# Kernel tuning notes

Measured on AMD Instinct MI355X. Metric: run time of the kernel, lower is better.

The kernel has to match this reference:

```python
import jax, jax.numpy as jnp
import numpy as np

B, T, I, H = 64, 188, 512, 1024
R = H  # recurrent_size == hidden_size (required for the cell math to be consistent)


def setup_inputs() -> dict:
    key = jax.random.key(0)
    ks = jax.random.split(key, 6)
    stdv = 1.0 / np.sqrt(H)
    u = lambda k, shape: jax.random.uniform(k, shape, jnp.float32, -stdv, stdv)
    return {
        "x": jax.random.normal(ks[0], (B, T, I), jnp.float32),
        "h0": jnp.zeros((B, R), jnp.float32),
        "c0": jnp.zeros((B, H), jnp.float32),
        "weight_ih": u(ks[1], (4 * H, I)),
        "weight_hh": u(ks[2], (4 * H, R)),
        "weight_rec": u(ks[3], (2 * R, H)),
        "bias": u(ks[4], (4 * H,)),
        "lengths": jax.random.randint(ks[5], (B,), 1, T + 1),
    }


def reference(x, h0, c0, weight_ih, weight_hh, weight_rec, bias, lengths):
    # length_matrix[j][t] == 1 iff t < lengths[j]; state is zeroed where 0
    mask = (jnp.arange(T)[:, None] < lengths[None, :]).astype(x.dtype)[:, :, None]  # [T,B,1]
    # precompute input projections for all timesteps: [T, B, 4H]
    pre_x = jnp.einsum('bti,gi->tbg', x, weight_ih) + bias

    def step(carry, inp):
        h, c = carry
        px, m = inp
        pre = px + h @ weight_hh.T           # [B, 4H]
        pre_c = c @ weight_rec.T             # [B, 2R] (peephole)
        i = jax.nn.sigmoid(pre[:, :H] + pre_c[:, :H])
        f = jax.nn.sigmoid(pre[:, H:2 * H] + pre_c[:, H:2 * H])
        g = jnp.tanh(pre[:, 2 * H:3 * H])
        c_new = f * c + i * g
        o = jax.nn.sigmoid(pre[:, 3 * H:] + c_new)
        h_new = o * jnp.tanh(c_new)
        h_new = h_new * m  # zero finished sequences (index_fill_ with 0)
        c_new = c_new * m
        return (h_new, c_new), (h_new, c_new)

    (_, _), (hs, cs) = jax.lax.scan(step, (h0, c0), (pre_x, mask))
    # stack over time then transpose(0,1) as in torch -> [B, T, H]
    return jnp.swapaxes(hs, 0, 1), jnp.swapaxes(cs, 0, 1)
```

## Files before the change

### kernel.cpp

```cpp
#include <hip/hip_runtime.h>


#define T_N 188

#define WS_PX     0UL
#define WS_XB     98566144UL
#define WS_WIHB   110886912UL
#define WS_WCOMB  115081216UL
#define WS_HST    127664128UL
#define WS_CST    127926272UL
#define WS_FLAGS  128188416UL
#define WS_WRECLO 128192512UL
#define WS_CSTLO  132386816UL

typedef __attribute__((ext_vector_type(8))) short short8;
typedef __attribute__((ext_vector_type(4))) float f4;

__device__ __forceinline__ float b2f(unsigned short u) {
    union { unsigned int i; float f; } v; v.i = ((unsigned int)u) << 16; return v.f;
}
__device__ __forceinline__ unsigned short f2b(float f) {
    unsigned int u = __float_as_uint(f);
    return (unsigned short)((u + 0x7FFFu + ((u >> 16) & 1u)) >> 16);
}
__device__ __forceinline__ float sigf(float x) { return 1.0f / (1.0f + __expf(-x)); }
__device__ __forceinline__ float tanh_(float x) {
    float e = __expf(2.0f * x); return 1.0f - 2.0f / (e + 1.0f);
}
#define MFMA(a, b, c) __builtin_amdgcn_mfma_f32_16x16x32_bf16((a), (b), (c), 0, 0, 0)

#define LD16(dst, addr) \
    asm volatile("global_load_dwordx4 %0, %1, off sc0 sc1" : "=&v"(dst) : "v"(addr))

__device__ __forceinline__ f4 px_init(const unsigned short* px, int t, int gate, int jg, int brow) {
    unsigned long long pv =
        *(const unsigned long long*)(px + ((long)(t * 4 + gate) * 1024 + jg) * 64 + brow);
    f4 r;
    r[0] = b2f((unsigned short)pv);
    r[1] = b2f((unsigned short)(pv >> 16));
    r[2] = b2f((unsigned short)(pv >> 32));
    r[3] = b2f((unsigned short)(pv >> 48));
    return r;
}

__global__ void k_prep(const float* __restrict__ x, const float* __restrict__ h0,
                       const float* __restrict__ c0, const float* __restrict__ wih,
                       const float* __restrict__ whh, const float* __restrict__ wrec,
                       unsigned short* __restrict__ xb, unsigned short* __restrict__ wihb,
                       unsigned short* __restrict__ wcomb, unsigned short* __restrict__ hst,
                       unsigned short* __restrict__ cst, unsigned short* __restrict__ wreclo,
                       unsigned short* __restrict__ cstlo, int* __restrict__ flags) {
    const long NX4 = 1540096, NWIH4 = 524288, NWHH4 = 1048576, NWREC4 = 524288, NH4 = 16384;
    const long total = NX4 + NWIH4 + NWHH4 + NWREC4 + NH4 + NH4;
    long gtid = (long)blockIdx.x * blockDim.x + threadIdx.x;
    for (long i = gtid; i < total; i += (long)gridDim.x * blockDim.x) {
        const float* src; unsigned short* dst; unsigned short* lo_dst = nullptr; long off = i;
        if (off < NX4)                   { src = x;    dst = xb; }
        else if ((off -= NX4) < NWIH4)   { src = wih;  dst = wihb; }
        else if ((off -= NWIH4) < NWHH4) { src = whh;  dst = wcomb; }
        else if ((off -= NWHH4) < NWREC4){ src = wrec; dst = wcomb + 4194304; lo_dst = wreclo; }
        else if ((off -= NWREC4) < NH4)  { src = h0;   dst = hst + 65536; }
        else { off -= NH4;                 src = c0;   dst = cst + 65536; lo_dst = cstlo + 65536; }
        float4 v = ((const float4*)src)[off];
        unsigned short hx = f2b(v.x), hy = f2b(v.y), hz = f2b(v.z), hw = f2b(v.w);
        unsigned long long o = (unsigned long long)hx
            | ((unsigned long long)hy << 16)
            | ((unsigned long long)hz << 32)
            | ((unsigned long long)hw << 48);
        *(unsigned long long*)(dst + off * 4) = o;
        if (lo_dst) {
            unsigned long long l = (unsigned long long)f2b(v.x - b2f(hx))
                | ((unsigned long long)f2b(v.y - b2f(hy)) << 16)
                | ((unsigned long long)f2b(v.z - b2f(hz)) << 32)
                | ((unsigned long long)f2b(v.w - b2f(hw)) << 48);
            *(unsigned long long*)(lo_dst + off * 4) = l;
        }
    }
    if (gtid < 1024) flags[gtid] = 0;
}

__global__ void __launch_bounds__(256) k_px(const unsigned short* __restrict__ xb,
                                            const unsigned short* __restrict__ wihb,
                                            const float* __restrict__ bias,
                                            unsigned short* __restrict__ px) {
    const int t = blockIdx.y;
    const int wv = threadIdx.x >> 6, lane = threadIdx.x & 63;
    const int col = lane & 15, quad = lane >> 4;
    const int n = blockIdx.x * 64 + wv * 16 + col;
    const float bn = bias[n];
    f4 acc[4];
#pragma unroll
    for (int mt = 0; mt < 4; ++mt) { acc[mt][0] = bn; acc[mt][1] = bn; acc[mt][2] = bn; acc[mt][3] = bn; }
    const unsigned short* bp = wihb + n * 512 + quad * 8;
#pragma unroll 4
    for (int kk = 0; kk < 16; ++kk) {
        short8 bf = *(const short8*)(bp + kk * 32);
#pragma unroll
        for (int mt = 0; mt < 4; ++mt) {
            const unsigned short* ap = xb + ((mt * 16 + col) * 188 + t) * 512 + kk * 32 + quad * 8;
            short8 af = *(const short8*)ap;
            acc[mt] = MFMA(af, bf, acc[mt]);
        }
    }
    const long pb = ((long)(t * 4 + (n >> 10)) * 1024 + (n & 1023)) * 64;
#pragma unroll
    for (int mt = 0; mt < 4; ++mt) {
        unsigned long long o = (unsigned long long)f2b(acc[mt][0])
            | ((unsigned long long)f2b(acc[mt][1]) << 16)
            | ((unsigned long long)f2b(acc[mt][2]) << 32)
            | ((unsigned long long)f2b(acc[mt][3]) << 48);
        *(unsigned long long*)(px + pb + mt * 16 + quad * 4) = o;
    }
}

__global__ void __launch_bounds__(256, 1) k_scan(
    const unsigned short* __restrict__ wcomb, const unsigned short* __restrict__ wreclo,
    const float* __restrict__ c0, const int* __restrict__ lengths,
    const unsigned short* __restrict__ px, unsigned short* __restrict__ hst,
    unsigned short* __restrict__ cst, unsigned short* __restrict__ cstlo,
    int* __restrict__ flags, float* __restrict__ out) {
    const int cu = blockIdx.x;
    const int g = cu >> 6, cig = cu & 63;
    const int jbase = cig * 16, b0 = g * 16;
    const int tid = threadIdx.x, wv = tid >> 6, lane = tid & 63;
    const int kh = wv >> 1, ts = wv & 1;
    const int kbase = kh * 512;
    const int col = lane & 15, quad = lane >> 4;

    __shared__ float pre[2][2][6][16][16];
    __shared__ float c_loc[16][16];

    short8 wf[4][16];
#pragma unroll
    for (int tile = 0; tile < 4; ++tile) {
        const unsigned short* src;
        if (ts == 0) {
            src = wcomb + (long)(tile * 1024 + jbase + col) * 1024 + kbase + quad * 8;
        } else if (tile < 2) {
            src = wcomb + (long)((4 + tile) * 1024 + jbase + col) * 1024 + kbase + quad * 8;
        } else {
            src = wreclo + (long)((tile - 2) * 1024 + jbase + col) * 1024 + kbase + quad * 8;
        }
#pragma unroll
        for (int kk = 0; kk < 16; ++kk) wf[tile][kk] = *(const short8*)(src + kk * 32);
    }
    {
        int b = tid >> 4, j = tid & 15;
        c_loc[b][j] = c0[(b0 + b) * 1024 + jbase + j];
    }
    const int my_len = lengths[b0 + (tid >> 4)];
    __syncthreads();

    float* out_h = out;
    float* out_c = out + 12320768;

    for (int t = 0; t < T_N; ++t) {
        const int sl_r = (t + 1) & 1, sl_w = t & 1, ps = t & 1;

        f4 pxv[4];
        if (ts == 0 && kh == 0) {
#pragma unroll
            for (int tile = 0; tile < 4; ++tile)
                pxv[tile] = px_init(px, t, tile, jbase + col, b0 + quad * 4);
        }

        if (t > 0) {
            if (wv == 0) {
                const int* fp = flags + g * 64 + lane;
                for (;;) {
                    int a = __hip_atomic_load(fp, __ATOMIC_RELAXED, __HIP_MEMORY_SCOPE_AGENT);
                    if (__all(a >= t)) break;
                    __builtin_amdgcn_s_sleep(1);
                }
            }
            __syncthreads();
            asm volatile("" ::: "memory");
        }

        const int sbase = sl_r * 65536 + (b0 + col) * 1024 + kbase + quad * 8;

        if (ts == 0) {
            const unsigned short* hp = hst + sbase;
            short8 hbuf[16];
#pragma unroll
            for (int kk = 0; kk < 16; ++kk) LD16(hbuf[kk], hp + kk * 32);
            f4 acc[4];
#pragma unroll
            for (int tile = 0; tile < 4; ++tile) {
                if (kh == 0) acc[tile] = pxv[tile];
                else { acc[tile][0] = 0.f; acc[tile][1] = 0.f; acc[tile][2] = 0.f; acc[tile][3] = 0.f; }
            }
            asm volatile("s_waitcnt vmcnt(0)" ::: "memory");
            __builtin_amdgcn_sched_barrier(0);
#pragma unroll
            for (int kk = 0; kk < 16; ++kk) {
                acc[0] = MFMA(hbuf[kk], wf[0][kk], acc[0]);
                acc[1] = MFMA(hbuf[kk], wf[1][kk], acc[1]);
                acc[2] = MFMA(hbuf[kk], wf[2][kk], acc[2]);
                acc[3] = MFMA(hbuf[kk], wf[3][kk], acc[3]);
            }
#pragma unroll
            for (int tile = 0; tile < 4; ++tile)
#pragma unroll
                for (int r = 0; r < 4; ++r) pre[ps][kh][tile][quad * 4 + r][col] = acc[tile][r];
        } else {
            const unsigned short* cph = cst + sbase;
            const unsigned short* cpl = cstlo + sbase;
            short8 chb[16], clb[16];
#pragma unroll
            for (int kk = 0; kk < 16; ++kk) LD16(chb[kk], cph + kk * 32);
#pragma unroll
            for (int kk = 0; kk < 16; ++kk) LD16(clb[kk], cpl + kk * 32);
            f4 a0 = {0.f, 0.f, 0.f, 0.f}, a1 = a0, a2 = a0, a3 = a0, a4 = a0, a5 = a0;
            asm volatile("s_waitcnt vmcnt(0)" ::: "memory");
            __builtin_amdgcn_sched_barrier(0);
#pragma unroll
            for (int kk = 0; kk < 16; ++kk) {
                a0 = MFMA(chb[kk], wf[0][kk], a0);
                a1 = MFMA(chb[kk], wf[1][kk], a1);
                a2 = MFMA(chb[kk], wf[2][kk], a2);
                a3 = MFMA(chb[kk], wf[3][kk], a3);
                a4 = MFMA(clb[kk], wf[0][kk], a4);
                a5 = MFMA(clb[kk], wf[1][kk], a5);
            }
#pragma unroll
            for (int r = 0; r < 4; ++r) {
                pre[ps][kh][4][quad * 4 + r][col] = a0[r] + a2[r] + a4[r];
                pre[ps][kh][5][quad * 4 + r][col] = a1[r] + a3[r] + a5[r];
            }
        }
        __syncthreads();

        float hn, cn; long ob;
        {
            const int b = tid >> 4, j = tid & 15;
            float pi = pre[ps][0][0][b][j] + pre[ps][1][0][b][j] + pre[ps][0][4][b][j] + pre[ps][1][4][b][j];
            float pf = pre[ps][0][1][b][j] + pre[ps][1][1][b][j] + pre[ps][0][5][b][j] + pre[ps][1][5][b][j];
            float pg = pre[ps][0][2][b][j] + pre[ps][1][2][b][j];
            float po = pre[ps][0][3][b][j] + pre[ps][1][3][b][j];
            const float cprev = c_loc[b][j];
            const float iv = sigf(pi), fv = sigf(pf), gv = tanh_(pg);
            cn = fv * cprev + iv * gv;
            float ov = sigf(po + cn);
            hn = ov * tanh_(cn);
            if (t >= my_len) { hn = 0.f; cn = 0.f; }
            c_loc[b][j] = cn;
            ob = (long)(b0 + b) * 192512 + (long)t * 1024 + jbase + j;
            const int sidx = sl_w * 65536 + (b0 + b) * 1024 + jbase + j;
            unsigned short hb  = f2b(hn);
            unsigned short chb2 = f2b(cn);
            unsigned short clb2 = f2b(cn - b2f(chb2));
            __hip_atomic_store(&hst[sidx],  hb,   __ATOMIC_RELAXED, __HIP_MEMORY_SCOPE_AGENT);
            __hip_atomic_store(&cst[sidx],  chb2, __ATOMIC_RELAXED, __HIP_MEMORY_SCOPE_AGENT);
            __hip_atomic_store(&cstlo[sidx], clb2, __ATOMIC_RELAXED, __HIP_MEMORY_SCOPE_AGENT);
        }
        asm volatile("s_waitcnt vmcnt(0)" ::: "memory");
        __syncthreads();
        if (tid == 0)
            __hip_atomic_store(&flags[cu], t + 1, __ATOMIC_RELAXED, __HIP_MEMORY_SCOPE_AGENT);
        out_h[ob] = hn;
        out_c[ob] = cn;
    }
}

extern "C" void kernel_launch(void* const* d_in, const int* in_sizes, int n_in,
                              void* d_out, int out_size, void* d_ws, size_t ws_size,
                              hipStream_t stream) {
    const float* x    = (const float*)d_in[0];
    const float* h0   = (const float*)d_in[1];
    const float* c0   = (const float*)d_in[2];
    const float* wih  = (const float*)d_in[3];
    const float* whh  = (const float*)d_in[4];
    const float* wrec = (const float*)d_in[5];
    const float* bias = (const float*)d_in[6];
    const int* lengths = (const int*)d_in[7];

    char* ws = (char*)d_ws;
    unsigned short* px     = (unsigned short*)(ws + WS_PX);
    unsigned short* xb     = (unsigned short*)(ws + WS_XB);
    unsigned short* wihb   = (unsigned short*)(ws + WS_WIHB);
    unsigned short* wcomb  = (unsigned short*)(ws + WS_WCOMB);
    unsigned short* hst    = (unsigned short*)(ws + WS_HST);
    unsigned short* cst    = (unsigned short*)(ws + WS_CST);
    unsigned short* wreclo = (unsigned short*)(ws + WS_WRECLO);
    unsigned short* cstlo  = (unsigned short*)(ws + WS_CSTLO);
    int* flags             = (int*)(ws + WS_FLAGS);
    float* out = (float*)d_out;

    hipLaunchKernelGGL(k_prep, dim3(2048), dim3(256), 0, stream,
                       x, h0, c0, wih, whh, wrec, xb, wihb, wcomb, hst, cst, wreclo, cstlo, flags);
    hipLaunchKernelGGL(k_px, dim3(64, 188), dim3(256), 0, stream, xb, wihb, bias, px);
    hipLaunchKernelGGL(k_scan, dim3(256), dim3(256), 0, stream,
                       wcomb, wreclo, c0, lengths, px, hst, cst, cstlo, flags, out);
}
```

Measured before the change: 1.666 ms.

## Use per-wave flags and all-wave polling to drop block barriers in scan

```diff
diff --git a/kernel.cpp b/kernel.cpp
--- a/kernel.cpp
+++ b/kernel.cpp
@@ -15,6 +15,7 @@
 
 typedef __attribute__((ext_vector_type(8))) short short8;
 typedef __attribute__((ext_vector_type(4))) float f4;
+typedef __attribute__((ext_vector_type(4))) int int4v;
 
 __device__ __forceinline__ float b2f(unsigned short u) {
     union { unsigned int i; float f; } v; v.i = ((unsigned int)u) << 16; return v.f;
@@ -33,8 +34,8 @@
     asm volatile("global_load_dwordx4 %0, %1, off sc0 sc1" : "=&v"(dst) : "v"(addr))
 
 __device__ __forceinline__ f4 px_init(const unsigned short* px, int t, int gate, int jg, int brow) {
-    unsigned long long pv =
-        *(const unsigned long long*)(px + ((long)(t * 4 + gate) * 1024 + jg) * 64 + brow);
+    unsigned long long pv = __builtin_nontemporal_load(
+        (const unsigned long long*)(px + ((long)(t * 4 + gate) * 1024 + jg) * 64 + brow));
     f4 r;
     r[0] = b2f((unsigned short)pv);
     r[1] = b2f((unsigned short)(pv >> 16));
@@ -126,9 +127,9 @@
     const int kh = wv >> 1, ts = wv & 1;
     const int kbase = kh * 512;
     const int col = lane & 15, quad = lane >> 4;
+    const int b_ = tid >> 4, j_ = tid & 15;
 
     __shared__ float pre[2][2][6][16][16];
-    __shared__ float c_loc[16][16];
 
     short8 wf[4][16];
 #pragma unroll
@@ -144,11 +145,9 @@
 #pragma unroll
         for (int kk = 0; kk < 16; ++kk) wf[tile][kk] = *(const short8*)(src + kk * 32);
     }
-    {
-        int b = tid >> 4, j = tid & 15;
-        c_loc[b][j] = c0[(b0 + b) * 1024 + jbase + j];
-    }
-    const int my_len = lengths[b0 + (tid >> 4)];
+    float c_reg = c0[(b0 + b_) * 1024 + jbase + j_];
+    const int my_len = lengths[b0 + b_];
+    float bal = (float)lane;
     __syncthreads();
 
     float* out_h = out;
@@ -165,15 +164,17 @@
         }
 
         if (t > 0) {
-            if (wv == 0) {
-                const int* fp = flags + g * 64 + lane;
-                for (;;) {
-                    int a = __hip_atomic_load(fp, __ATOMIC_RELAXED, __HIP_MEMORY_SCOPE_AGENT);
-                    if (__all(a >= t)) break;
-                    __builtin_amdgcn_s_sleep(1);
-                }
-            }
-            __syncthreads();
+            const int* fp = flags + g * 256 + lane * 4;
+            for (;;) {
+                int4v fv;
+                asm volatile("global_load_dwordx4 %0, %1, off sc0 sc1" : "=&v"(fv) : "v"(fp));
+                asm volatile("s_waitcnt vmcnt(0)" ::: "memory");
+                int m0 = fv[0] < fv[1] ? fv[0] : fv[1];
+                int m1 = fv[2] < fv[3] ? fv[2] : fv[3];
+                int m = m0 < m1 ? m0 : m1;
+                if (__all(m >= t)) break;
+                bal = __builtin_fmaf(bal, 1.000001f, 1e-7f);
+            }
             asm volatile("" ::: "memory");
         }
 
@@ -231,36 +232,36 @@
         }
         __syncthreads();
 
-        float hn, cn; long ob;
+        float hn, cn;
         {
-            const int b = tid >> 4, j = tid & 15;
-            float pi = pre[ps][0][0][b][j] + pre[ps][1][0][b][j] + pre[ps][0][4][b][j] + pre[ps][1][4][b][j];
-            float pf = pre[ps][0][1][b][j] + pre[ps][1][1][b][j] + pre[ps][0][5][b][j] + pre[ps][1][5][b][j];
-            float pg = pre[ps][0][2][b][j] + pre[ps][1][2][b][j];
-            float po = pre[ps][0][3][b][j] + pre[ps][1][3][b][j];
-            const float cprev = c_loc[b][j];
+            float pi = pre[ps][0][0][b_][j_] + pre[ps][1][0][b_][j_] + pre[ps][0][4][b_][j_] + pre[ps][1][4][b_][j_];
+            float pf = pre[ps][0][1][b_][j_] + pre[ps][1][1][b_][j_] + pre[ps][0][5][b_][j_] + pre[ps][1][5][b_][j_];
+            float pg = pre[ps][0][2][b_][j_] + pre[ps][1][2][b_][j_];
+            float po = pre[ps][0][3][b_][j_] + pre[ps][1][3][b_][j_];
+            const float cprev = c_reg;
             const float iv = sigf(pi), fv = sigf(pf), gv = tanh_(pg);
             cn = fv * cprev + iv * gv;
             float ov = sigf(po + cn);
             hn = ov * tanh_(cn);
             if (t >= my_len) { hn = 0.f; cn = 0.f; }
-            c_loc[b][j] = cn;
-            ob = (long)(b0 + b) * 192512 + (long)t * 1024 + jbase + j;
-            const int sidx = sl_w * 65536 + (b0 + b) * 1024 + jbase + j;
-            unsigned short hb  = f2b(hn);
+            c_reg = cn;
+            const int sidx = sl_w * 65536 + (b0 + b_) * 1024 + jbase + j_;
+            unsigned short hb   = f2b(hn);
             unsigned short chb2 = f2b(cn);
             unsigned short clb2 = f2b(cn - b2f(chb2));
-            __hip_atomic_store(&hst[sidx],  hb,   __ATOMIC_RELAXED, __HIP_MEMORY_SCOPE_AGENT);
-            __hip_atomic_store(&cst[sidx],  chb2, __ATOMIC_RELAXED, __HIP_MEMORY_SCOPE_AGENT);
+            __hip_atomic_store(&hst[sidx],   hb,   __ATOMIC_RELAXED, __HIP_MEMORY_SCOPE_AGENT);
+            __hip_atomic_store(&cst[sidx],   chb2, __ATOMIC_RELAXED, __HIP_MEMORY_SCOPE_AGENT);
             __hip_atomic_store(&cstlo[sidx], clb2, __ATOMIC_RELAXED, __HIP_MEMORY_SCOPE_AGENT);
         }
         asm volatile("s_waitcnt vmcnt(0)" ::: "memory");
-        __syncthreads();
-        if (tid == 0)
-            __hip_atomic_store(&flags[cu], t + 1, __ATOMIC_RELAXED, __HIP_MEMORY_SCOPE_AGENT);
-        out_h[ob] = hn;
-        out_c[ob] = cn;
-    }
+        if (lane == 0)
+            __hip_atomic_store(&flags[g * 256 + cig * 4 + wv], t + 1,
+                               __ATOMIC_RELAXED, __HIP_MEMORY_SCOPE_AGENT);
+        const long ob = (long)(b0 + b_) * 192512 + (long)t * 1024 + jbase + j_;
+        __builtin_nontemporal_store(hn, out_h + ob);
+        __builtin_nontemporal_store(cn, out_c + ob);
+    }
+    asm volatile("" :: "v"(bal));
 }
 
 extern "C" void kernel_launch(void* const* d_in, const int* in_sizes, int n_in,
```

After: 2.519 ms. +51.2%, slower.
